# Kernel tuning notes

Hardware: AMD Instinct MI355X
Metric: run time of the kernel (lower is better)

Reference implementation:

```python
import jax, jax.numpy as jnp
import numpy as np

B, RULE_DIM, E, P, TOP_K = 8192, 128, 64, 16, 3
EPS = 1e-5
CONF_THRESH = 0.1


def _ln(x, g, b):
    # torch.nn.LayerNorm: biased variance, eps=1e-5
    m = x.mean(-1, keepdims=True)
    v = ((x - m) ** 2).mean(-1, keepdims=True)
    return (x - m) / jnp.sqrt(v + EPS) * g + b


def setup_inputs() -> dict:
    key = jax.random.key(0)
    ks = jax.random.split(key, 8)
    s = lambda fan: 1.0 / np.sqrt(fan)
    return {
        "rule_embedding": jax.random.normal(ks[0], (B, RULE_DIM), jnp.float32),
        "rp_w1": jax.random.normal(ks[1], (RULE_DIM, 256), jnp.float32) * s(RULE_DIM),
        "rp_b1": jnp.zeros((256,), jnp.float32),
        "rp_g1": jnp.ones((256,), jnp.float32),
        "rp_be1": jnp.zeros((256,), jnp.float32),
        "rp_w2": jax.random.normal(ks[2], (256, 512), jnp.float32) * s(256),
        "rp_b2": jnp.zeros((512,), jnp.float32),
        "rp_g2": jnp.ones((512,), jnp.float32),
        "rp_be2": jnp.zeros((512,), jnp.float32),
        "op_w": jax.random.normal(ks[3], (512, E), jnp.float32) * s(512),
        "op_b": jnp.zeros((E,), jnp.float32),
        "pe_w1": jax.random.normal(ks[4], (E, 512, 256), jnp.float32) * s(512),
        "pe_b1": jnp.zeros((E, 256), jnp.float32),
        "pe_g": jnp.ones((E, 256), jnp.float32),
        "pe_beta": jnp.zeros((E, 256), jnp.float32),
        "pe_w2": jax.random.normal(ks[5], (E, 256, P), jnp.float32) * s(256),
        "pe_b2": jnp.zeros((E, P), jnp.float32),
    }


def reference(rule_embedding, rp_w1, rp_b1, rp_g1, rp_be1, rp_w2, rp_b2,
              rp_g2, rp_be2, op_w, op_b, pe_w1, pe_b1, pe_g, pe_beta,
              pe_w2, pe_b2):
    # rule_parser: Linear -> LN -> ReLU -> Linear -> LN -> ReLU
    h = jax.nn.relu(_ln(rule_embedding @ rp_w1 + rp_b1, rp_g1, rp_be1))   # [B,256]
    features = jax.nn.relu(_ln(h @ rp_w2 + rp_b2, rp_g2, rp_be2))         # [B,512]

    # op routing: softmax + top-k
    op_probs = jax.nn.softmax(features @ op_w + op_b, axis=-1)            # [B,E]
    top_probs, top_idx = jax.lax.top_k(op_probs, TOP_K)                   # [B,K]

    # per-op param predictor MLP, evaluated for every expert (vmap over E)
    def expert(w1, b1, g, be, w2, b2):
        z = jax.nn.relu(_ln(features @ w1 + b1, g, be))                   # [B,256]
        return z @ w2 + b2                                                # [B,P]

    h2_all = jax.vmap(expert)(pe_w1, pe_b1, pe_g, pe_beta, pe_w2, pe_b2)  # [E,B,P]

    # gather the selected expert's raw param logits per (token, slot)
    params_sel = h2_all[top_idx, jnp.arange(B)[:, None], :]               # [B,K,P]

    # original skips ops with confidence < 0.1 -> mask them out
    mask = (top_probs >= CONF_THRESH).astype(params_sel.dtype)            # [B,K]
    params_out = params_sel * mask[..., None]

    return top_probs, top_idx, params_out
```

## Files before the change

kernel.cpp:

```cpp
#include <hip/hip_runtime.h>
#include <math.h>

#define Bv   8192
#define EPSv 1e-5f
#define CONFv 0.1f
#define MB (1024*1024)

typedef __attribute__((ext_vector_type(8))) short short8;
typedef __attribute__((ext_vector_type(4))) float f32x4;

__device__ __forceinline__ float wave_sum64(float v){
  #pragma unroll
  for (int o = 32; o; o >>= 1) v += __shfl_xor(v, o, 64);
  return v;
}

__device__ __forceinline__ void split3f(float x, short &h, short &m, short &l){
  unsigned u = __float_as_uint(x);
  h = (short)(u >> 16);
  float r1 = x - __uint_as_float(u & 0xffff0000u);
  unsigned u1 = __float_as_uint(r1);
  m = (short)(u1 >> 16);
  float r2 = r1 - __uint_as_float(u1 & 0xffff0000u);
  l = (short)(__float_as_uint(r2) >> 16);
}

__device__ __forceinline__ void split2f(float x, short &h, short &m){
  unsigned u = __float_as_uint(x);
  h = (short)(u >> 16);
  float r1 = x - __uint_as_float(u & 0xffff0000u);
  m = (short)(__float_as_uint(r1) >> 16);
}

__device__ __forceinline__ f32x4 mfma5(short8 ah, short8 am,
                                       short8 bh, short8 bm, short8 bl, f32x4 c){
  c = __builtin_amdgcn_mfma_f32_16x16x32_bf16(am, bm, c, 0, 0, 0);
  c = __builtin_amdgcn_mfma_f32_16x16x32_bf16(ah, bl, c, 0, 0, 0);
  c = __builtin_amdgcn_mfma_f32_16x16x32_bf16(am, bh, c, 0, 0, 0);
  c = __builtin_amdgcn_mfma_f32_16x16x32_bf16(ah, bm, c, 0, 0, 0);
  c = __builtin_amdgcn_mfma_f32_16x16x32_bf16(ah, bh, c, 0, 0, 0);
  return c;
}

__device__ __forceinline__ f32x4 mfma3(short8 ah, short8 al,
                                       short8 bh, short8 bl, f32x4 c){
  c = __builtin_amdgcn_mfma_f32_16x16x32_bf16(al, bh, c, 0, 0, 0);
  c = __builtin_amdgcn_mfma_f32_16x16x32_bf16(ah, bl, c, 0, 0, 0);
  c = __builtin_amdgcn_mfma_f32_16x16x32_bf16(ah, bh, c, 0, 0, 0);
  return c;
}

__global__ __launch_bounds__(256) void k_pre(
    const float* __restrict__ w1, const float* __restrict__ w2,
    const float* __restrict__ opw,
    unsigned short* __restrict__ w1p, unsigned short* __restrict__ w2p,
    unsigned short* __restrict__ opwp, int* __restrict__ cnt)
{
  int bid = blockIdx.x;
  if (bid < 128){
    int gid = bid*256 + threadIdx.x;
    int k = gid >> 8, n = gid & 255;
    short h, m, l;
    split3f(w1[gid], h, m, l);
    int idx = (((n >> 4)*4 + (k >> 5))*64 + (((k >> 3) & 3)*16 + (n & 15)))*8 + (k & 7);
    w1p[idx]             = (unsigned short)h;
    w1p[32768 + idx]     = (unsigned short)m;
    w1p[2*32768 + idx]   = (unsigned short)l;
  } else if (bid < 640){
    int gid = (bid - 128)*256 + threadIdx.x;
    int k = gid >> 9, n = gid & 511;
    short h, m, l;
    split3f(w2[gid], h, m, l);
    int idx = (((n >> 4)*8 + (k >> 5))*64 + (((k >> 3) & 3)*16 + (n & 15)))*8 + (k & 7);
    w2p[idx]             = (unsigned short)h;
    w2p[131072 + idx]    = (unsigned short)m;
    w2p[2*131072 + idx]  = (unsigned short)l;
  } else if (bid < 768){
    int gid = (bid - 640)*256 + threadIdx.x;
    int k = gid >> 6, n = gid & 63;
    short h, m, l;
    split3f(opw[gid], h, m, l);
    int idx = (((n >> 4)*16 + (k >> 5))*64 + (((k >> 3) & 3)*16 + (n & 15)))*8 + (k & 7);
    opwp[idx]            = (unsigned short)h;
    opwp[32768 + idx]    = (unsigned short)m;
    opwp[2*32768 + idx]  = (unsigned short)l;
  } else {
    if (threadIdx.x < 64) cnt[threadIdx.x] = 0;
  }
}

__global__ __launch_bounds__(1024) void k_fused(const float* __restrict__ X,
    const unsigned short* __restrict__ w1p, const float* __restrict__ b1,
    const float* __restrict__ g1, const float* __restrict__ be1,
    const unsigned short* __restrict__ w2p, const float* __restrict__ b2,
    const float* __restrict__ g2, const float* __restrict__ be2,
    const unsigned short* __restrict__ opwp, const float* __restrict__ opb,
    unsigned short* __restrict__ fh, unsigned short* __restrict__ fl,
    float* __restrict__ dout, int* __restrict__ cnt, int* __restrict__ list,
    const float* __restrict__ pw1, const float* __restrict__ pw2,
    unsigned short* __restrict__ p1, unsigned short* __restrict__ p2)
{
  extern __shared__ unsigned char smem[];

  if (blockIdx.x >= 256){
    int pb = blockIdx.x - 256;
    if (pb < 1024){
      int t = pb*1024 + threadIdx.x;
      int e = t >> 14, rem = t & 16383, kg = rem >> 8, n = rem & 255;
      const float* src = pw1 + ((size_t)e << 17) + (size_t)(kg*8)*256 + n;
      short8 h, l;
      #pragma unroll
      for (int j = 0; j < 8; j++){
        float w = src[(size_t)j*256];
        unsigned u = __float_as_uint(w);
        float r2 = w - __uint_as_float(u & 0xffff0000u);
        h[j] = (short)(u >> 16);
        l[j] = (short)(__float_as_uint(r2) >> 16);
      }
      int idx8 = ((((n >> 4)*16 + (kg >> 2))*64) + (kg & 3)*16 + (n & 15)) << 3;
      unsigned short* ep = p1 + (size_t)e * 262144;
      *(short8*)(ep + idx8)          = h;
      *(short8*)(ep + 131072 + idx8) = l;
    } else {
      int t = (pb - 1024)*1024 + threadIdx.x;
      int e = t >> 9, rem = t & 511, kg = rem >> 4, n = rem & 15;
      const float* src = pw2 + (size_t)e*4096 + (size_t)(kg*8)*16 + n;
      short8 h, l;
      #pragma unroll
      for (int j = 0; j < 8; j++){
        float w = src[(size_t)j*16];
        unsigned u = __float_as_uint(w);
        float r2 = w - __uint_as_float(u & 0xffff0000u);
        h[j] = (short)(u >> 16);
        l[j] = (short)(__float_as_uint(r2) >> 16);
      }
      int idx8 = (((kg >> 2)*64) + (kg & 3)*16 + n) << 3;
      unsigned short* ep = p2 + (size_t)e * 8192;
      *(short8*)(ep + idx8)        = h;
      *(short8*)(ep + 4096 + idx8) = l;
    }
    return;
  }

  unsigned short* xh  = (unsigned short*)smem;
  unsigned short* xm  = xh + 4096;
  unsigned short* hbh = xh + 8192;
  unsigned short* hbm = xh + 16384;
  unsigned short* gah = xh;
  unsigned short* gam = xh + 16384;
  __shared__ float ps[32][20];
  __shared__ float pq[32][20];
  __shared__ float mi[32][2];
  __shared__ float lg[32][64];

  const int tid = threadIdx.x;
  const int r0  = blockIdx.x * 32;
  const int wave = tid >> 6, lane = tid & 63, lquad = lane >> 4, l15 = lane & 15;

  {
    int r = tid >> 5, c4 = tid & 31;
    float4 v = ((const float4*)X)[(size_t)(r0+r)*32 + c4];
    unsigned u0 = __float_as_uint(v.x), u1 = __float_as_uint(v.y);
    unsigned u2 = __float_as_uint(v.z), u3 = __float_as_uint(v.w);
    float m0 = v.x - __uint_as_float(u0 & 0xffff0000u);
    float m1 = v.y - __uint_as_float(u1 & 0xffff0000u);
    float m2 = v.z - __uint_as_float(u2 & 0xffff0000u);
    float m3 = v.w - __uint_as_float(u3 & 0xffff0000u);
    unsigned hp0 = (u0 >> 16) | (u1 & 0xffff0000u);
    unsigned hp1 = (u2 >> 16) | (u3 & 0xffff0000u);
    unsigned mp0 = (__float_as_uint(m0) >> 16) | (__float_as_uint(m1) & 0xffff0000u);
    unsigned mp1 = (__float_as_uint(m2) >> 16) | (__float_as_uint(m3) & 0xffff0000u);
    int gk = c4 >> 1, half = c4 & 1;
    int off = r*128 + ((gk ^ (r & 7)) << 3) + half*4;
    ((unsigned*)(xh + off))[0] = hp0;
    ((unsigned*)(xh + off))[1] = hp1;
    ((unsigned*)(xm + off))[0] = mp0;
    ((unsigned*)(xm + off))[1] = mp1;
  }
  __syncthreads();

  float bcol1, gcol1, becol1;
  {
    int col = wave*16 + l15;
    bcol1 = b1[col]; gcol1 = g1[col]; becol1 = be1[col];
  }
  {
    f32x4 acc[2];
    acc[0] = (f32x4){0.f,0.f,0.f,0.f};
    acc[1] = (f32x4){0.f,0.f,0.f,0.f};
    const int pstride = 32768;
    for (int ks4 = 0; ks4 < 4; ks4++){
      const unsigned short* bp = w1p + (((wave*4 + ks4)*64 + lane) << 3);
      short8 bh = *(const short8*)bp;
      short8 bm = *(const short8*)(bp + pstride);
      short8 bl = *(const short8*)(bp + 2*pstride);
      #pragma unroll
      for (int mt = 0; mt < 2; mt++){
        int r = mt*16 + l15;
        int off = r*128 + (((ks4*4 + lquad) ^ (r & 7)) << 3);
        short8 ah = *(const short8*)(xh + off);
        short8 am = *(const short8*)(xm + off);
        acc[mt] = mfma5(ah, am, bh, bm, bl, acc[mt]);
      }
    }
    #pragma unroll
    for (int mt = 0; mt < 2; mt++)
      #pragma unroll
      for (int reg = 0; reg < 4; reg++){
        float z = acc[mt][reg] + bcol1;
        float s = z, q = z*z;
        #pragma unroll
        for (int o = 1; o < 16; o <<= 1){ s += __shfl_xor(s, o, 64); q += __shfl_xor(q, o, 64); }
        int row = mt*16 + lquad*4 + reg;
        if (l15 == 0){ ps[row][wave] = s; pq[row][wave] = q; }
      }
    __syncthreads();
    if (tid < 32){
      int row = tid;
      float4 s0 = *(const float4*)&ps[row][0],  s1 = *(const float4*)&ps[row][4];
      float4 s2 = *(const float4*)&ps[row][8],  s3 = *(const float4*)&ps[row][12];
      float4 q0 = *(const float4*)&pq[row][0],  q1 = *(const float4*)&pq[row][4];
      float4 q2 = *(const float4*)&pq[row][8],  q3 = *(const float4*)&pq[row][12];
      float s = s0.x; s += s0.y; s += s0.z; s += s0.w;
      s += s1.x; s += s1.y; s += s1.z; s += s1.w;
      s += s2.x; s += s2.y; s += s2.z; s += s2.w;
      s += s3.x; s += s3.y; s += s3.z; s += s3.w;
      float q = q0.x; q += q0.y; q += q0.z; q += q0.w;
      q += q1.x; q += q1.y; q += q1.z; q += q1.w;
      q += q2.x; q += q2.y; q += q2.z; q += q2.w;
      q += q3.x; q += q3.y; q += q3.z; q += q3.w;
      float mean = s * (1.0f/256.0f);
      float var  = q * (1.0f/256.0f) - mean*mean;
      mi[row][0] = mean;
      mi[row][1] = 1.0f / sqrtf(var + EPSv);
    }
    __syncthreads();
    #pragma unroll
    for (int mt = 0; mt < 2; mt++)
      #pragma unroll
      for (int reg = 0; reg < 4; reg++){
        int row = mt*16 + lquad*4 + reg;
        float2 mv = *(const float2*)mi[row];
        int col = wave*16 + l15;
        float z = acc[mt][reg] + bcol1;
        float y = fmaxf((z - mv.x)*mv.y*gcol1 + becol1, 0.f);
        short hh, mm2;
        split2f(y, hh, mm2);
        int gg = col >> 3, c7 = col & 7;
        int adr = row*256 + ((gg ^ (row & 7)) << 3) + c7;
        hbh[adr] = (unsigned short)hh;
        hbm[adr] = (unsigned short)mm2;
      }
  }
  __syncthreads();

  f32x4 acc2[2][2];
  #pragma unroll
  for (int mt = 0; mt < 2; mt++)
    #pragma unroll
    for (int nt = 0; nt < 2; nt++) acc2[mt][nt] = (f32x4){0.f,0.f,0.f,0.f};
  {
    const int pstride = 131072;
    for (int ks4 = 0; ks4 < 8; ks4++){
      short8 ah[2], am[2];
      #pragma unroll
      for (int mt = 0; mt < 2; mt++){
        int r = mt*16 + l15;
        int off = r*256 + (((ks4*4 + lquad) ^ (r & 7)) << 3);
        ah[mt] = *(const short8*)(hbh + off);
        am[mt] = *(const short8*)(hbm + off);
      }
      #pragma unroll
      for (int nt = 0; nt < 2; nt++){
        int ntg = wave*2 + nt;
        const unsigned short* bp = w2p + (((ntg*8 + ks4)*64 + lane) << 3);
        short8 bh = *(const short8*)bp;
        short8 bm = *(const short8*)(bp + pstride);
        short8 bl = *(const short8*)(bp + 2*pstride);
        #pragma unroll
        for (int mt = 0; mt < 2; mt++)
          acc2[mt][nt] = mfma5(ah[mt], am[mt], bh, bm, bl, acc2[mt][nt]);
      }
    }
  }

  float bcol[2], gcol[2], becol[2];
  #pragma unroll
  for (int nt = 0; nt < 2; nt++){
    int col = (wave*2 + nt)*16 + l15;
    bcol[nt] = b2[col]; gcol[nt] = g2[col]; becol[nt] = be2[col];
  }
  #pragma unroll
  for (int mt = 0; mt < 2; mt++)
    #pragma unroll
    for (int reg = 0; reg < 4; reg++){
      float s = 0.f, q = 0.f;
      #pragma unroll
      for (int nt = 0; nt < 2; nt++){
        float z = acc2[mt][nt][reg] + bcol[nt];
        s += z; q += z*z;
      }
      #pragma unroll
      for (int o = 1; o < 16; o <<= 1){ s += __shfl_xor(s, o, 64); q += __shfl_xor(q, o, 64); }
      int row = mt*16 + lquad*4 + reg;
      if (l15 == 0){ ps[row][wave] = s; pq[row][wave] = q; }
    }
  __syncthreads();
  if (tid < 32){
    int row = tid;
    float4 s0 = *(const float4*)&ps[row][0],  s1 = *(const float4*)&ps[row][4];
    float4 s2 = *(const float4*)&ps[row][8],  s3 = *(const float4*)&ps[row][12];
    float4 q0 = *(const float4*)&pq[row][0],  q1 = *(const float4*)&pq[row][4];
    float4 q2 = *(const float4*)&pq[row][8],  q3 = *(const float4*)&pq[row][12];
    float s = s0.x; s += s0.y; s += s0.z; s += s0.w;
    s += s1.x; s += s1.y; s += s1.z; s += s1.w;
    s += s2.x; s += s2.y; s += s2.z; s += s2.w;
    s += s3.x; s += s3.y; s += s3.z; s += s3.w;
    float q = q0.x; q += q0.y; q += q0.z; q += q0.w;
    q += q1.x; q += q1.y; q += q1.z; q += q1.w;
    q += q2.x; q += q2.y; q += q2.z; q += q2.w;
    q += q3.x; q += q3.y; q += q3.z; q += q3.w;
    float mean = s * (1.0f/512.0f);
    float var  = q * (1.0f/512.0f) - mean*mean;
    mi[row][0] = mean;
    mi[row][1] = 1.0f / sqrtf(var + EPSv);
  }
  __syncthreads();

  #pragma unroll
  for (int mt = 0; mt < 2; mt++)
    #pragma unroll
    for (int reg = 0; reg < 4; reg++){
      int row = mt*16 + lquad*4 + reg;
      float2 mv = *(const float2*)mi[row];
      #pragma unroll
      for (int nt = 0; nt < 2; nt++){
        int col = (wave*2 + nt)*16 + l15;
        float z = acc2[mt][nt][reg] + bcol[nt];
        float y = fmaxf((z - mv.x)*mv.y*gcol[nt] + becol[nt], 0.f);
        short hh, mm2;
        split2f(y, hh, mm2);
        int gg = col >> 3, c7 = col & 7;
        int adr = row*512 + ((gg ^ (row & 7)) << 3) + c7;
        gah[adr] = (unsigned short)hh;
        gam[adr] = (unsigned short)mm2;
      }
    }
  __syncthreads();

  if (wave < 4){
    f32x4 accg[2];
    accg[0] = (f32x4){0.f,0.f,0.f,0.f};
    accg[1] = (f32x4){0.f,0.f,0.f,0.f};
    for (int kt = 0; kt < 16; kt++){
      const unsigned short* bp = opwp + (((wave*16 + kt)*64 + lane) << 3);
      short8 bh = *(const short8*)bp;
      short8 bm = *(const short8*)(bp + 32768);
      short8 bl = *(const short8*)(bp + 65536);
      #pragma unroll
      for (int mt = 0; mt < 2; mt++){
        int r = mt*16 + l15;
        int off = r*512 + (((kt*4 + lquad) ^ (r & 7)) << 3);
        short8 ah = *(const short8*)(gah + off);
        short8 am = *(const short8*)(gam + off);
        accg[mt] = mfma5(ah, am, bh, bm, bl, accg[mt]);
      }
    }
    float opbv = opb[wave*16 + l15];
    #pragma unroll
    for (int mt = 0; mt < 2; mt++)
      #pragma unroll
      for (int reg = 0; reg < 4; reg++)
        lg[mt*16 + lquad*4 + reg][wave*16 + l15] = accg[mt][reg] + opbv;
  } else {
    int t4 = (wave - 4)*64 + lane;
    for (int i = t4; i < 4096; i += 768){
      int p = i >> 11, rem = i & 2047, r = rem >> 6, gg = rem & 63;
      short8 v = *(const short8*)((p ? gam : gah) + r*512 + ((gg ^ (r & 7)) << 3));
      unsigned short* dst = (p ? fl : fh) + (size_t)(r0 + r)*512 + gg*8;
      *(short8*)dst = v;
    }
  }
  __syncthreads();

  {
    for (int rr = 0; rr < 2; rr++){
      int r = wave*2 + rr, row = r0 + r;
      float l = lg[r][lane];
      float mx = l;
      #pragma unroll
      for (int o = 32; o; o >>= 1) mx = fmaxf(mx, __shfl_xor(mx, o, 64));
      float p = expf(l - mx);
      float s = wave_sum64(p);
      p /= s;
      float pv = p;
      for (int j = 0; j < 3; j++){
        float v = pv; int idx = lane;
        #pragma unroll
        for (int o = 32; o; o >>= 1){
          float ov = __shfl_xor(v, o, 64);
          int   oi = __shfl_xor(idx, o, 64);
          if (ov > v || (ov == v && oi < idx)){ v = ov; idx = oi; }
        }
        if (lane == 0){
          dout[(size_t)row*3 + j]                = v;
          dout[(size_t)Bv*3 + (size_t)row*3 + j] = (float)idx;
        }
        if (v >= CONFv){
          if (lane == 0){
            int pos = atomicAdd(&cnt[idx], 1);
            list[idx*Bv + pos] = (row << 2) | j;
          }
        } else {
          if (lane < 16) dout[(size_t)Bv*6 + (size_t)row*48 + j*16 + lane] = 0.f;
        }
        if (lane == idx) pv = -1.0f;
      }
    }
  }
}

__global__ __launch_bounds__(1024) void k_expert(const unsigned short* __restrict__ fh,
    const unsigned short* __restrict__ fl,
    const unsigned short* __restrict__ p1, const float* __restrict__ b1,
    const float* __restrict__ g,  const float* __restrict__ beta,
    const unsigned short* __restrict__ p2, const float* __restrict__ b2,
    const int* __restrict__ cnt,  const int* __restrict__ list,
    float* __restrict__ dout)
{
  __shared__ unsigned short xbuf[65536];
  unsigned short* xh = xbuf;
  unsigned short* xl = xbuf + 32768;
  unsigned short* zp = xbuf;
  __shared__ float ps[64][16];
  __shared__ float pq[64][16];
  __shared__ float mi[64][2];
  __shared__ int sdesc[3];

  const int tid = threadIdx.x;
  const int wave = tid >> 6, lane = tid & 63;
  const int lquad = lane >> 4, l15 = lane & 15;

  if (wave == 0){
    int c  = cnt[lane];
    int tl = (c + 63) >> 6;
    int incl = tl;
    #pragma unroll
    for (int o = 1; o < 64; o <<= 1){
      int v = __shfl_up(incl, o, 64);
      if (lane >= o) incl += v;
    }
    int total = __shfl(incl, 63, 64);
    int G   = (total + 7) >> 3;
    int grp = blockIdx.x & 7, rr = blockIdx.x >> 3;
    int lgc = grp*G + rr;
    int ok  = (G > 0) && (rr < G) && (lgc < total);
    unsigned long long bm = __ballot(ok && (incl > lgc));
    if (lane == 0){
      if (!ok || bm == 0ull){ sdesc[0] = -1; }
      else {
        int e = __ffsll((long long)bm) - 1;
        sdesc[0] = e; sdesc[1] = lgc; sdesc[2] = 0;
      }
    }
    if (bm != 0ull && ok){
      int e = __ffsll((long long)bm) - 1;
      int excl = __shfl(incl - tl, e, 64);
      int ne   = __shfl(c, e, 64);
      if (lane == 0){ sdesc[1] = lgc - excl; sdesc[2] = ne; }
    }
  }
  __syncthreads();
  const int e = sdesc[0];
  if (e < 0) return;
  const int t = sdesc[1];
  const int n = sdesc[2];
  const int base = t * 64;
  const int m = min(64, n - base);
  const int* lrow = list + e*Bv + base;

  for (int i = tid; i < 8192; i += 1024){
    int p = i >> 12, rem = i & 4095, r = rem >> 6, gg = rem & 63;
    int ev = lrow[(r < m) ? r : 0];
    int row = ev >> 2;
    const unsigned short* src = (p ? fl : fh) + (size_t)row*512 + gg*8;
    short8 v = *(const short8*)src;
    unsigned short* dst = (p ? xl : xh) + r*512 + ((gg ^ (r & 7)) << 3);
    *(short8*)dst = v;
  }
  __syncthreads();

  const unsigned short* p1e = p1 + (size_t)e * 262144;
  f32x4 acc[4];
  #pragma unroll
  for (int mt = 0; mt < 4; mt++) acc[mt] = (f32x4){0.f,0.f,0.f,0.f};

  for (int kt = 0; kt < 16; kt++){
    const unsigned short* bp = p1e + (((wave*16 + kt)*64 + lane) << 3);
    short8 bh = *(const short8*)bp;
    short8 bl = *(const short8*)(bp + 131072);
    int gk = kt*4 + lquad;
    #pragma unroll
    for (int mt = 0; mt < 4; mt++){
      int r = mt*16 + l15;
      int off = r*512 + ((gk ^ (r & 7)) << 3);
      short8 ah = *(const short8*)(xh + off);
      short8 al = *(const short8*)(xl + off);
      acc[mt] = mfma3(ah, al, bh, bl, acc[mt]);
    }
  }

  float bb, gv, bv;
  {
    int col = wave*16 + l15;
    bb = b1[e*256 + col];
    gv = g[e*256 + col];
    bv = beta[e*256 + col];
  }
  #pragma unroll
  for (int mt = 0; mt < 4; mt++)
    #pragma unroll
    for (int reg = 0; reg < 4; reg++){
      float z = acc[mt][reg] + bb;
      float s = z, q = z*z;
      #pragma unroll
      for (int o = 1; o < 16; o <<= 1){ s += __shfl_xor(s, o, 64); q += __shfl_xor(q, o, 64); }
      int row = mt*16 + lquad*4 + reg;
      if (l15 == 0){ ps[row][wave] = s; pq[row][wave] = q; }
    }
  __syncthreads();
  if (tid < 64){
    int row = tid;
    float s = 0.f, q = 0.f;
    #pragma unroll
    for (int c4 = 0; c4 < 4; c4++){
      float4 sv = *(const float4*)&ps[row][c4*4];
      float4 qv = *(const float4*)&pq[row][c4*4];
      s += sv.x + sv.y + sv.z + sv.w;
      q += qv.x + qv.y + qv.z + qv.w;
    }
    float mean = s * (1.0f/256.0f);
    float var  = q * (1.0f/256.0f) - mean*mean;
    mi[row][0] = mean;
    mi[row][1] = 1.0f / sqrtf(var + EPSv);
  }
  __syncthreads();

  #pragma unroll
  for (int mt = 0; mt < 4; mt++)
    #pragma unroll
    for (int reg = 0; reg < 4; reg++){
      int row = mt*16 + lquad*4 + reg;
      float2 mv = *(const float2*)mi[row];
      int col = wave*16 + l15;
      float z = acc[mt][reg] + bb;
      float y = fmaxf((z - mv.x)*mv.y*gv + bv, 0.f);
      short hh, mm2;
      split2f(y, hh, mm2);
      zp[row*528 + col]       = (unsigned short)hh;
      zp[row*528 + 264 + col] = (unsigned short)mm2;
    }
  __syncthreads();

  if (wave < 4){
    const unsigned short* p2e = p2 + (size_t)e * 8192;
    f32x4 acc2 = (f32x4){0.f,0.f,0.f,0.f};
    for (int kt2 = 0; kt2 < 8; kt2++){
      const unsigned short* zb = zp + (wave*16 + l15)*528 + kt2*32 + lquad*8;
      short8 ahh = *(const short8*)zb;
      short8 all2 = *(const short8*)(zb + 264);
      const unsigned short* bp = p2e + ((kt2*64 + lane) << 3);
      short8 bh = *(const short8*)bp;
      short8 bl = *(const short8*)(bp + 4096);
      acc2 = mfma3(ahh, all2, bh, bl, acc2);
    }
    float b2v = b2[e*16 + l15];
    #pragma unroll
    for (int reg = 0; reg < 4; reg++){
      int rl = wave*16 + lquad*4 + reg;
      if (rl < m){
        int ev = lrow[rl];
        int row = ev >> 2, j = ev & 3;
        dout[(size_t)Bv*6 + (size_t)row*48 + j*16 + l15] = acc2[reg] + b2v;
      }
    }
  }
}

extern "C" void kernel_launch(void* const* d_in, const int* in_sizes, int n_in,
                              void* d_out, int out_size, void* d_ws, size_t ws_size,
                              hipStream_t stream)
{
  const float* X   = (const float*)d_in[0];
  const float* w1  = (const float*)d_in[1];
  const float* b1  = (const float*)d_in[2];
  const float* g1  = (const float*)d_in[3];
  const float* be1 = (const float*)d_in[4];
  const float* w2  = (const float*)d_in[5];
  const float* b2  = (const float*)d_in[6];
  const float* g2  = (const float*)d_in[7];
  const float* be2 = (const float*)d_in[8];
  const float* opw = (const float*)d_in[9];
  const float* opb = (const float*)d_in[10];
  const float* pw1 = (const float*)d_in[11];
  const float* pb1 = (const float*)d_in[12];
  const float* pg  = (const float*)d_in[13];
  const float* pbe = (const float*)d_in[14];
  const float* pw2 = (const float*)d_in[15];
  const float* pb2 = (const float*)d_in[16];
  float* out = (float*)d_out;
  char*  ws  = (char*)d_ws;

  unsigned short* p1E    = (unsigned short*)ws;
  unsigned short* p2E    = (unsigned short*)(ws + (size_t)32*MB);
  unsigned short* w1p_rp = (unsigned short*)(ws + (size_t)33*MB);
  unsigned short* w2p_rp = (unsigned short*)(ws + (size_t)34*MB);
  unsigned short* opwp   = (unsigned short*)(ws + (size_t)35*MB);
  unsigned short* fh     = (unsigned short*)(ws + (size_t)36*MB);
  unsigned short* fl     = (unsigned short*)(ws + (size_t)44*MB);
  int*            list   = (int*)(ws + (size_t)52*MB);
  int*            cnt    = (int*)(ws + (size_t)54*MB);

  k_pre   <<<769, 256, 0, stream>>>(w1, w2, opw, w1p_rp, w2p_rp, opwp, cnt);
  k_fused <<<1312, 1024, 65536, stream>>>(X, w1p_rp, b1, g1, be1,
                                          w2p_rp, b2, g2, be2, opwp, opb,
                                          fh, fl, out, cnt, list,
                                          pw1, pw2, p1E, p2E);
  k_expert<<<448, 1024, 0, stream>>>(fh, fl, p1E, pb1, pg, pbe, p2E, pb2,
                                     cnt, list, out);
}
```

Measured before the change: 169.9 us.

## Split expert W1 to bf16 hi/lo inside expert kernel instead of prepass

Removes the separate pass that converted all 64 expert W1 matrices (32 MB of fp32) into packed bf16 hi/lo buffers. The expert kernel now reads fp32 W1 directly and splits it into hi/lo bf16 in registers right before the MFMAs. The small W2 conversion moves from the fused kernel into the prepass kernel, so the fused kernel only launches its 256 compute blocks. This avoids writing and re-reading the packed W1 copy, but each expert tile now issues strided scalar fp32 loads and repeats the split work for every tile of tokens routed to the same expert.

```diff
diff --git a/kernel.cpp b/kernel.cpp
--- a/kernel.cpp
+++ b/kernel.cpp
@@ -52,9 +52,10 @@
 
 __global__ __launch_bounds__(256) void k_pre(
     const float* __restrict__ w1, const float* __restrict__ w2,
-    const float* __restrict__ opw,
+    const float* __restrict__ opw, const float* __restrict__ pw2,
     unsigned short* __restrict__ w1p, unsigned short* __restrict__ w2p,
-    unsigned short* __restrict__ opwp, int* __restrict__ cnt)
+    unsigned short* __restrict__ opwp, unsigned short* __restrict__ p2,
+    int* __restrict__ cnt)
 {
   int bid = blockIdx.x;
   if (bid < 128){
@@ -84,6 +85,23 @@
     opwp[idx]            = (unsigned short)h;
     opwp[32768 + idx]    = (unsigned short)m;
     opwp[2*32768 + idx]  = (unsigned short)l;
+  } else if (bid < 896){
+    int t = (bid - 768)*256 + threadIdx.x;
+    int e = t >> 9, rem = t & 511, kg = rem >> 4, n = rem & 15;
+    const float* src = pw2 + (size_t)e*4096 + (size_t)(kg*8)*16 + n;
+    short8 h, l;
+    #pragma unroll
+    for (int j = 0; j < 8; j++){
+      float w = src[(size_t)j*16];
+      unsigned u = __float_as_uint(w);
+      float r2 = w - __uint_as_float(u & 0xffff0000u);
+      h[j] = (short)(u >> 16);
+      l[j] = (short)(__float_as_uint(r2) >> 16);
+    }
+    int idx8 = (((kg >> 2)*64) + (kg & 3)*16 + n) << 3;
+    unsigned short* ep = p2 + (size_t)e * 8192;
+    *(short8*)(ep + idx8)        = h;
+    *(short8*)(ep + 4096 + idx8) = l;
   } else {
     if (threadIdx.x < 64) cnt[threadIdx.x] = 0;
   }
@@ -96,52 +114,9 @@
     const float* __restrict__ g2, const float* __restrict__ be2,
     const unsigned short* __restrict__ opwp, const float* __restrict__ opb,
     unsigned short* __restrict__ fh, unsigned short* __restrict__ fl,
-    float* __restrict__ dout, int* __restrict__ cnt, int* __restrict__ list,
-    const float* __restrict__ pw1, const float* __restrict__ pw2,
-    unsigned short* __restrict__ p1, unsigned short* __restrict__ p2)
+    float* __restrict__ dout, int* __restrict__ cnt, int* __restrict__ list)
 {
   extern __shared__ unsigned char smem[];
-
-  if (blockIdx.x >= 256){
-    int pb = blockIdx.x - 256;
-    if (pb < 1024){
-      int t = pb*1024 + threadIdx.x;
-      int e = t >> 14, rem = t & 16383, kg = rem >> 8, n = rem & 255;
-      const float* src = pw1 + ((size_t)e << 17) + (size_t)(kg*8)*256 + n;
-      short8 h, l;
-      #pragma unroll
-      for (int j = 0; j < 8; j++){
-        float w = src[(size_t)j*256];
-        unsigned u = __float_as_uint(w);
-        float r2 = w - __uint_as_float(u & 0xffff0000u);
-        h[j] = (short)(u >> 16);
-        l[j] = (short)(__float_as_uint(r2) >> 16);
-      }
-      int idx8 = ((((n >> 4)*16 + (kg >> 2))*64) + (kg & 3)*16 + (n & 15)) << 3;
-      unsigned short* ep = p1 + (size_t)e * 262144;
-      *(short8*)(ep + idx8)          = h;
-      *(short8*)(ep + 131072 + idx8) = l;
-    } else {
-      int t = (pb - 1024)*1024 + threadIdx.x;
-      int e = t >> 9, rem = t & 511, kg = rem >> 4, n = rem & 15;
-      const float* src = pw2 + (size_t)e*4096 + (size_t)(kg*8)*16 + n;
-      short8 h, l;
-      #pragma unroll
-      for (int j = 0; j < 8; j++){
-        float w = src[(size_t)j*16];
-        unsigned u = __float_as_uint(w);
-        float r2 = w - __uint_as_float(u & 0xffff0000u);
-        h[j] = (short)(u >> 16);
-        l[j] = (short)(__float_as_uint(r2) >> 16);
-      }
-      int idx8 = (((kg >> 2)*64) + (kg & 3)*16 + n) << 3;
-      unsigned short* ep = p2 + (size_t)e * 8192;
-      *(short8*)(ep + idx8)        = h;
-      *(short8*)(ep + 4096 + idx8) = l;
-    }
-    return;
-  }
-
   unsigned short* xh  = (unsigned short*)smem;
   unsigned short* xm  = xh + 4096;
   unsigned short* hbh = xh + 8192;
@@ -422,7 +397,7 @@
 
 __global__ __launch_bounds__(1024) void k_expert(const unsigned short* __restrict__ fh,
     const unsigned short* __restrict__ fl,
-    const unsigned short* __restrict__ p1, const float* __restrict__ b1,
+    const float* __restrict__ pw1, const float* __restrict__ b1,
     const float* __restrict__ g,  const float* __restrict__ beta,
     const unsigned short* __restrict__ p2, const float* __restrict__ b2,
     const int* __restrict__ cnt,  const int* __restrict__ list,
@@ -490,15 +465,24 @@
   }
   __syncthreads();
 
-  const unsigned short* p1e = p1 + (size_t)e * 262144;
+  const float* bw = pw1 + (size_t)e*131072 + wave*16 + l15;
   f32x4 acc[4];
   #pragma unroll
   for (int mt = 0; mt < 4; mt++) acc[mt] = (f32x4){0.f,0.f,0.f,0.f};
 
   for (int kt = 0; kt < 16; kt++){
-    const unsigned short* bp = p1e + (((wave*16 + kt)*64 + lane) << 3);
-    short8 bh = *(const short8*)bp;
-    short8 bl = *(const short8*)(bp + 131072);
+    const float* bk = bw + (size_t)(kt*32 + lquad*8)*256;
+    float wv[8];
+    #pragma unroll
+    for (int j = 0; j < 8; j++) wv[j] = bk[(size_t)j*256];
+    short8 bh, bl;
+    #pragma unroll
+    for (int j = 0; j < 8; j++){
+      unsigned u = __float_as_uint(wv[j]);
+      float r2 = wv[j] - __uint_as_float(u & 0xffff0000u);
+      bh[j] = (short)(u >> 16);
+      bl[j] = (short)(__float_as_uint(r2) >> 16);
+    }
     int gk = kt*4 + lquad;
     #pragma unroll
     for (int mt = 0; mt < 4; mt++){
@@ -611,7 +595,6 @@
   float* out = (float*)d_out;
   char*  ws  = (char*)d_ws;
 
-  unsigned short* p1E    = (unsigned short*)ws;
   unsigned short* p2E    = (unsigned short*)(ws + (size_t)32*MB);
   unsigned short* w1p_rp = (unsigned short*)(ws + (size_t)33*MB);
   unsigned short* w2p_rp = (unsigned short*)(ws + (size_t)34*MB);
@@ -621,11 +604,11 @@
   int*            list   = (int*)(ws + (size_t)52*MB);
   int*            cnt    = (int*)(ws + (size_t)54*MB);
 
-  k_pre   <<<769, 256, 0, stream>>>(w1, w2, opw, w1p_rp, w2p_rp, opwp, cnt);
-  k_fused <<<1312, 1024, 65536, stream>>>(X, w1p_rp, b1, g1, be1,
-                                          w2p_rp, b2, g2, be2, opwp, opb,
-                                          fh, fl, out, cnt, list,
-                                          pw1, pw2, p1E, p2E);
-  k_expert<<<448, 1024, 0, stream>>>(fh, fl, p1E, pb1, pg, pbe, p2E, pb2,
+  k_pre   <<<897, 256, 0, stream>>>(w1, w2, opw, pw2,
+                                    w1p_rp, w2p_rp, opwp, p2E, cnt);
+  k_fused <<<256, 1024, 65536, stream>>>(X, w1p_rp, b1, g1, be1,
+                                         w2p_rp, b2, g2, be2, opwp, opb,
+                                         fh, fl, out, cnt, list);
+  k_expert<<<448, 1024, 0, stream>>>(fh, fl, pw1, pb1, pg, pbe, p2E, pb2,
                                      cnt, list, out);
 }
```

Measured after the change: 164.2 us, median of 2. 1.03x faster.
